# Performance work log

Hardware: AMD Instinct MI355X
Metric: run time of the kernel (lower is better)

Reference implementation:

```python
import jax, jax.numpy as jnp
import numpy as np
import math

N, E, B, T = 100000, 500000, 4096, 12
IN, HID, H = 64, 32, 4
HC = HID * H  # 128
ED = 4


def setup_inputs() -> dict:
    key = jax.random.key(0)
    ks = jax.random.split(key, 40)
    w = lambda k, shape: jax.random.normal(k, shape, jnp.float32) * 0.05
    inp = {
        'x': jax.random.normal(ks[0], (N, IN), jnp.float32),
        'edge_index': jax.random.randint(ks[1], (2, E), 0, N, jnp.int32),
        'edge_attr': jax.random.normal(ks[2], (E, ED), jnp.float32),
        'batch': jnp.sort(jax.random.randint(ks[3], (N,), 0, B, jnp.int32)),
        'r_target': jax.random.randint(ks[4], (B,), 0, T, jnp.int32),
        # layer 1 (in=IN)
        'Wq1': w(ks[5], (IN, HC)), 'bq1': w(ks[6], (HC,)),
        'Wk1': w(ks[7], (IN, HC)), 'bk1': w(ks[8], (HC,)),
        'Wv1': w(ks[9], (IN, HC)), 'bv1': w(ks[10], (HC,)),
        'We1': w(ks[11], (ED, HC)),
        'Ws1': w(ks[12], (IN, HC)), 'bs1': w(ks[13], (HC,)),
        # layers 2 and 3 stacked (in=HC)
        'Wq23': w(ks[14], (2, HC, HC)), 'bq23': w(ks[15], (2, HC)),
        'Wk23': w(ks[16], (2, HC, HC)), 'bk23': w(ks[17], (2, HC)),
        'Wv23': w(ks[18], (2, HC, HC)), 'bv23': w(ks[19], (2, HC)),
        'We23': w(ks[20], (2, ED, HC)),
        'Ws23': w(ks[21], (2, HC, HC)), 'bs23': w(ks[22], (2, HC)),
        # per-task linear heads (out_channels=1)
        'head_W': w(ks[23], (T, HC)), 'head_b': w(ks[24], (T,)),
    }
    return inp


def tconv(x, src, dst, ea, Wq, bq, Wk, bk, Wv, bv, We, Ws, bs):
    """PyG TransformerConv: gather -> per-edge MHA score -> segment softmax -> scatter."""
    q = (x @ Wq + bq).reshape(-1, H, HID)   # [N,H,C]
    k = (x @ Wk + bk).reshape(-1, H, HID)
    v = (x @ Wv + bv).reshape(-1, H, HID)
    e = (ea @ We).reshape(-1, H, HID)       # [E,H,C] (lin_edge has no bias)
    kj = k[src] + e                          # [E,H,C]
    alpha = (q[dst] * kj).sum(-1) / math.sqrt(HID)          # [E,H]
    amax = jax.ops.segment_max(alpha, dst, num_segments=N)  # [N,H]
    alpha = jnp.exp(alpha - amax[dst])
    asum = jax.ops.segment_sum(alpha, dst, num_segments=N)
    alpha = alpha / (asum[dst] + 1e-16)
    msg = (v[src] + e) * alpha[..., None]                   # [E,H,C]
    out = jax.ops.segment_sum(msg, dst, num_segments=N).reshape(N, HC)
    return out + x @ Ws + bs                 # root_weight skip connection


def reference(x, edge_index, edge_attr, batch, r_target,
              Wq1, bq1, Wk1, bk1, Wv1, bv1, We1, Ws1, bs1,
              Wq23, bq23, Wk23, bk23, Wv23, bv23, We23, Ws23, bs23,
              head_W, head_b):
    src, dst = edge_index[0], edge_index[1]
    h = jax.nn.relu(tconv(x, src, dst, edge_attr, Wq1, bq1, Wk1, bk1, Wv1, bv1, We1, Ws1, bs1))
    h = jax.nn.relu(tconv(h, src, dst, edge_attr, Wq23[0], bq23[0], Wk23[0], bk23[0], Wv23[0], bv23[0], We23[0], Ws23[0], bs23[0]))
    h = tconv(h, src, dst, edge_attr, Wq23[1], bq23[1], Wk23[1], bk23[1], Wv23[1], bv23[1], We23[1], Ws23[1], bs23[1])
    # global mean pool per graph
    cnt = jax.ops.segment_sum(jnp.ones((N,), h.dtype), batch, num_segments=B)
    pooled = jax.ops.segment_sum(h, batch, num_segments=B) / jnp.maximum(cnt, 1.0)[:, None]  # [B,HC]
    # dropout p=0.3 is a no-op in eval mode
    # per-task head selected by r_target (out_channels=1, squeezed)
    return (pooled * head_W[r_target]).sum(-1) + head_b[r_target]  # [B]
```

## Files before the change

kernel.cpp:

```cpp
#include <hip/hip_runtime.h>
#include <hip/hip_bf16.h>

#define NN 100000
#define EE 500000
#define BB 4096
#define HC 128
#define SCAN_ELEM 1024
#define NSB ((NN + SCAN_ELEM - 1) / SCAN_ELEM)

typedef __bf16 bf16_t;
typedef bf16_t bf16x8 __attribute__((ext_vector_type(8)));
typedef float f32x4 __attribute__((ext_vector_type(4)));
typedef float f32x2 __attribute__((ext_vector_type(2)));

__device__ __forceinline__ unsigned short f2bf(float f) {
    unsigned u = __builtin_bit_cast(unsigned, f);
    u += 0x7FFFu + ((u >> 16) & 1u);
    return (unsigned short)(u >> 16);
}
__device__ __forceinline__ float bflo(unsigned u) {
    return __builtin_bit_cast(float, u << 16);
}
__device__ __forceinline__ float bfhi(unsigned u) {
    return __builtin_bit_cast(float, u & 0xFFFF0000u);
}
__device__ __forceinline__ f32x2 unpk2(unsigned u) {
    return (f32x2){ bflo(u), bfhi(u) };
}

__global__ __launch_bounds__(256) void conv_x(const float* __restrict__ in,
                                              unsigned short* __restrict__ outb,
                                              int total4)
{
    const int g = blockIdx.x * 256 + threadIdx.x;
    if (g >= total4) return;
    const float4 f = *(const float4*)(in + (size_t)g * 4);
    ushort4 u;
    u.x = f2bf(f.x); u.y = f2bf(f.y); u.z = f2bf(f.z); u.w = f2bf(f.w);
    *(ushort4*)(outb + (size_t)g * 4) = u;
}

__global__ __launch_bounds__(256) void prep_w(
    const float* __restrict__ Wq, const float* __restrict__ Wk,
    const float* __restrict__ Wv, const float* __restrict__ Ws,
    unsigned short* __restrict__ Wt, int K)
{
    const int g = blockIdx.x * 256 + threadIdx.x;
    const int per = K * 128;
    if (g >= 4 * per) return;
    const int p = g / per, r = g - p * per;
    const int k = r >> 7, n = r & 127;
    const float* W = p == 0 ? Wq : p == 1 ? Wk : p == 2 ? Wv : Ws;
    Wt[(size_t)p * per + (size_t)n * K + k] = f2bf(W[k * 128 + n]);
}

template<int NKT>
__global__ __launch_bounds__(256) void gemm_mfma(
    const unsigned short* __restrict__ A,
    const unsigned short* __restrict__ Wt,
    const float* __restrict__ bq, const float* __restrict__ bk,
    const float* __restrict__ bv, const float* __restrict__ bs,
    unsigned* __restrict__ Qb, unsigned* __restrict__ KVb,
    float* __restrict__ S)
{
    constexpr int K = NKT * 32;
    const int lane = threadIdx.x & 63;
    const int p = threadIdx.x >> 6;
    const int m = lane & 15, kq = lane >> 4;
    const int rows0 = blockIdx.x * 32;

    const unsigned short* Wp = Wt + (size_t)p * 128 * K;
    const float* bias = p == 0 ? bq : p == 1 ? bk : p == 2 ? bv : bs;

    bf16x8 a[2][NKT];
#pragma unroll
    for (int mt = 0; mt < 2; mt++)
#pragma unroll
        for (int kt = 0; kt < NKT; kt++)
            a[mt][kt] = *(const bf16x8*)(A + (size_t)(rows0 + mt * 16 + m) * K + kt * 32 + kq * 8);

    f32x4 acc[2][8];
#pragma unroll
    for (int mt = 0; mt < 2; mt++)
#pragma unroll
        for (int nt = 0; nt < 8; nt++)
            acc[mt][nt] = (f32x4){0.f, 0.f, 0.f, 0.f};

#pragma unroll
    for (int nt = 0; nt < 8; nt++) {
#pragma unroll
        for (int kt = 0; kt < NKT; kt++) {
            const bf16x8 b = *(const bf16x8*)(Wp + (size_t)(nt * 16 + m) * K + kt * 32 + kq * 8);
            acc[0][nt] = __builtin_amdgcn_mfma_f32_16x16x32_bf16(a[0][kt], b, acc[0][nt], 0, 0, 0);
            acc[1][nt] = __builtin_amdgcn_mfma_f32_16x16x32_bf16(a[1][kt], b, acc[1][nt], 0, 0, 0);
        }
    }

    if (p == 3) {
#pragma unroll
        for (int nt = 0; nt < 8; nt++) {
            const float bi = bias[nt * 16 + m];
#pragma unroll
            for (int mt = 0; mt < 2; mt++) {
                float* o = S + (size_t)(rows0 + mt * 16 + kq * 4) * HC + nt * 16 + m;
#pragma unroll
                for (int r = 0; r < 4; r++) o[r * HC] = acc[mt][nt][r] + bi;
            }
        }
    } else {
        unsigned* out = p == 0 ? Qb : (p == 1 ? KVb : KVb + 64);
        const int stride = p == 0 ? 64 : 128;
#pragma unroll
        for (int nt = 0; nt < 8; nt++) {
            const float bi = bias[nt * 16 + m];
#pragma unroll
            for (int mt = 0; mt < 2; mt++) {
#pragma unroll
                for (int r = 0; r < 4; r++) {
                    const float v0 = acc[mt][nt][r] + bi;
                    const float v1 = __shfl_xor(v0, 1);
                    if (!(m & 1)) {
                        const unsigned pk = (unsigned)f2bf(v0) | ((unsigned)f2bf(v1) << 16);
                        out[(size_t)(rows0 + mt * 16 + kq * 4 + r) * stride + nt * 8 + (m >> 1)] = pk;
                    }
                }
            }
        }
    }
}

__global__ __launch_bounds__(256) void deg_k(const int* __restrict__ ei, int* __restrict__ deg)
{
    const int e = blockIdx.x * 256 + threadIdx.x;
    if (e < EE) atomicAdd(&deg[ei[EE + e]], 1);
}

__global__ __launch_bounds__(256) void scan_part(const int* __restrict__ deg,
                                                 int* __restrict__ bsum)
{
    __shared__ int red[256];
    const int base = blockIdx.x * SCAN_ELEM + threadIdx.x * 4;
    int s = 0;
#pragma unroll
    for (int j = 0; j < 4; j++) { const int i = base + j; if (i < NN) s += deg[i]; }
    red[threadIdx.x] = s;
    __syncthreads();
    for (int st = 128; st > 0; st >>= 1) {
        if (threadIdx.x < st) red[threadIdx.x] += red[threadIdx.x + st];
        __syncthreads();
    }
    if (threadIdx.x == 0) bsum[blockIdx.x] = red[0];
}

__global__ __launch_bounds__(128) void scan_top(const int* __restrict__ bsum,
                                                int* __restrict__ boff)
{
    __shared__ int buf[128];
    const int v = (threadIdx.x < NSB) ? bsum[threadIdx.x] : 0;
    buf[threadIdx.x] = v;
    __syncthreads();
    for (int s = 1; s < 128; s <<= 1) {
        const int t = (threadIdx.x >= s) ? buf[threadIdx.x - s] : 0;
        __syncthreads();
        buf[threadIdx.x] += t;
        __syncthreads();
    }
    if (threadIdx.x < NSB) boff[threadIdx.x] = buf[threadIdx.x] - v;
}

__global__ __launch_bounds__(256) void scan_final(const int* __restrict__ deg,
                                                  const int* __restrict__ boff,
                                                  int* __restrict__ off,
                                                  int* __restrict__ cursor)
{
    __shared__ int tsum[256];
    const int base = blockIdx.x * SCAN_ELEM + threadIdx.x * 4;
    int vals[4];
    int s = 0;
#pragma unroll
    for (int j = 0; j < 4; j++) {
        const int i = base + j;
        vals[j] = (i < NN) ? deg[i] : 0;
        s += vals[j];
    }
    tsum[threadIdx.x] = s;
    __syncthreads();
    for (int st = 1; st < 256; st <<= 1) {
        const int t = (threadIdx.x >= st) ? tsum[threadIdx.x - st] : 0;
        __syncthreads();
        tsum[threadIdx.x] += t;
        __syncthreads();
    }
    int ex = boff[blockIdx.x] + tsum[threadIdx.x] - s;
#pragma unroll
    for (int j = 0; j < 4; j++) {
        const int i = base + j;
        if (i < NN) { off[i] = ex; cursor[i] = ex; }
        ex += vals[j];
    }
    if (blockIdx.x == NSB - 1 && threadIdx.x == 255)
        off[NN] = boff[blockIdx.x] + tsum[255];
}

__global__ __launch_bounds__(256) void bucket_k(const int* __restrict__ ei,
                                                const float* __restrict__ ea,
                                                int* __restrict__ cursor,
                                                int* __restrict__ esrc,
                                                float4* __restrict__ eaf)
{
    const int e = blockIdx.x * 256 + threadIdx.x;
    if (e < EE) {
        const int d = ei[EE + e];
        const int p = atomicAdd(&cursor[d], 1);
        esrc[p] = ei[e];
        eaf[p] = *(const float4*)(ea + (size_t)e * 4);
    }
}

__global__ __launch_bounds__(256) void cnt_k(const int* __restrict__ batch,
                                             float* __restrict__ cnt)
{
    const int n = blockIdx.x * 256 + threadIdx.x;
    if (n < NN) atomicAdd(&cnt[batch[n]], 1.0f);
}

__global__ __launch_bounds__(256) void edge_fused(
    const int* __restrict__ esrc, const float4* __restrict__ eaf,
    const float* __restrict__ We,
    const unsigned* __restrict__ Qb, const unsigned* __restrict__ KVb,
    const int* __restrict__ off, const float* __restrict__ S,
    unsigned short* __restrict__ Hb,
    const int* __restrict__ batch, float* __restrict__ pooled,
    int fuse_pool)
{
    const int lane = threadIdx.x & 63;
    const int slot = lane >> 4;
    const int c8   = lane & 15;
    const int cb   = c8 * 8;
    const int ceq  = cb + slot * 2;
    const int n = blockIdx.x * 4 + (threadIdx.x >> 6);

    const int beg = off[n], end = off[n + 1];

    const float2 sk2 = *(const float2*)(S + (size_t)n * HC + ceq);
    const uint4 qv = *(const uint4*)(Qb + (size_t)n * 64 + c8 * 4);
    f32x2 q2[4];
    q2[0] = unpk2(qv.x); q2[1] = unpk2(qv.y);
    q2[2] = unpk2(qv.z); q2[3] = unpk2(qv.w);

    float qep[4];
#pragma unroll
    for (int d = 0; d < 4; d++) {
        const float4 wa = *(const float4*)(We + d * HC + cb);
        const float4 wb = *(const float4*)(We + d * HC + cb + 4);
        qep[d] = wa.x * q2[0].x + wa.y * q2[0].y + wa.z * q2[1].x + wa.w * q2[1].y
               + wb.x * q2[2].x + wb.y * q2[2].y + wb.z * q2[3].x + wb.w * q2[3].y;
    }

    f32x2 num2[4] = {(f32x2){0.f, 0.f}, (f32x2){0.f, 0.f},
                     (f32x2){0.f, 0.f}, (f32x2){0.f, 0.f}};
    f32x4 s4 = (f32x4){0.f, 0.f, 0.f, 0.f};
    float den = 0.f;

    auto COMPUTE = [&](const uint4& ku, const uint4& vu, const float4& ac, bool act) {
        f32x2 t2 = q2[0] * unpk2(ku.x);
        t2 += q2[1] * unpk2(ku.y);
        t2 += q2[2] * unpk2(ku.z);
        t2 += q2[3] * unpk2(ku.w);
        float tot = t2.x + t2.y
                  + ac.x * qep[0] + ac.y * qep[1] + ac.z * qep[2] + ac.w * qep[3];
        tot += __shfl_xor(tot, 1);
        tot += __shfl_xor(tot, 2);
        float al = __expf(tot * 0.17677669529663687f);
        if (!act) al = 0.f;
        num2[0] += unpk2(vu.x) * al;
        num2[1] += unpk2(vu.y) * al;
        num2[2] += unpk2(vu.z) * al;
        num2[3] += unpk2(vu.w) * al;
        s4.x += ac.x * al; s4.y += ac.y * al;
        s4.z += ac.z * al; s4.w += ac.w * al;
        den += al;
    };

    if (beg < end) {
        const int e1 = end - 1;
        int p0 = beg + slot; if (p0 > e1) p0 = e1;
        const int srcA = esrc[p0];
        const float4 aA = eaf[p0];
        const unsigned* kvA = KVb + (size_t)srcA * 128 + c8 * 4;
        const uint4 kA = *(const uint4*)kvA;
        const uint4 vA = *(const uint4*)(kvA + 64);
        if (beg + 4 < end) {
            int p1 = beg + 4 + slot; if (p1 > e1) p1 = e1;
            const int srcB = esrc[p1];
            float4 aB = eaf[p1];
            const unsigned* kvB = KVb + (size_t)srcB * 128 + c8 * 4;
            uint4 kB = *(const uint4*)kvB;
            uint4 vB = *(const uint4*)(kvB + 64);
            COMPUTE(kA, vA, aA, true);
            int base = beg + 4;
            for (;;) {
                if (base + 4 < end) {
                    int pn = base + 4 + slot; if (pn > e1) pn = e1;
                    const int srcN = esrc[pn];
                    const float4 aN = eaf[pn];
                    COMPUTE(kB, vB, aB, (base + slot) < end);
                    const unsigned* kvN = KVb + (size_t)srcN * 128 + c8 * 4;
                    kB = *(const uint4*)kvN;
                    vB = *(const uint4*)(kvN + 64);
                    aB = aN;
                    base += 4;
                } else {
                    COMPUTE(kB, vB, aB, (base + slot) < end);
                    break;
                }
            }
        } else {
            COMPUTE(kA, vA, aA, (beg + slot) < end);
        }
    }

#pragma unroll
    for (int j = 0; j < 4; j++) {
        num2[j].x += __shfl_xor(num2[j].x, 16);
        num2[j].y += __shfl_xor(num2[j].y, 16);
        num2[j].x += __shfl_xor(num2[j].x, 32);
        num2[j].y += __shfl_xor(num2[j].y, 32);
    }
    s4.x += __shfl_xor(s4.x, 16); s4.y += __shfl_xor(s4.y, 16);
    s4.z += __shfl_xor(s4.z, 16); s4.w += __shfl_xor(s4.w, 16);
    s4.x += __shfl_xor(s4.x, 32); s4.y += __shfl_xor(s4.y, 32);
    s4.z += __shfl_xor(s4.z, 32); s4.w += __shfl_xor(s4.w, 32);
    den += __shfl_xor(den, 16);
    den += __shfl_xor(den, 32);
    const float inv = 1.f / (den + 1e-16f);

    f32x2 mynum = slot == 0 ? num2[0] : slot == 1 ? num2[1]
                : slot == 2 ? num2[2] : num2[3];
    float ev0 = 0.f, ev1 = 0.f;
#pragma unroll
    for (int d = 0; d < 4; d++) {
        const float2 wd = *(const float2*)(We + d * HC + ceq);
        const float sd = d == 0 ? s4.x : d == 1 ? s4.y : d == 2 ? s4.z : s4.w;
        ev0 += sd * wd.x;
        ev1 += sd * wd.y;
    }
    const float o0 = (mynum.x + ev0) * inv + sk2.x;
    const float o1 = (mynum.y + ev1) * inv + sk2.y;

    if (!fuse_pool) {
        const float r0 = fmaxf(o0, 0.f), r1 = fmaxf(o1, 0.f);
        const unsigned pk = (unsigned)f2bf(r0) | ((unsigned)f2bf(r1) << 16);
        *(unsigned*)(Hb + (size_t)n * HC + ceq) = pk;
    } else {
        const int b = batch[n];
        atomicAdd(pooled + (size_t)b * HC + ceq,     o0);
        atomicAdd(pooled + (size_t)b * HC + ceq + 1, o1);
    }
}

__global__ __launch_bounds__(256) void head_k(
    const float* __restrict__ pooled, const float* __restrict__ cnt,
    const int* __restrict__ rt, const float* __restrict__ hW,
    const float* __restrict__ hb, float* __restrict__ out)
{
    const int lane = threadIdx.x & 63;
    const int b = blockIdx.x * 4 + (threadIdx.x >> 6);
    if (b >= BB) return;
    const int t = rt[b];
    const int c = lane * 2;
    const float2 p2 = *(const float2*)(pooled + (size_t)b * HC + c);
    const float2 w2 = *(const float2*)(hW + (size_t)t * HC + c);
    float part = p2.x * w2.x + p2.y * w2.y;
    part += __shfl_xor(part, 1);
    part += __shfl_xor(part, 2);
    part += __shfl_xor(part, 4);
    part += __shfl_xor(part, 8);
    part += __shfl_xor(part, 16);
    part += __shfl_xor(part, 32);
    if (lane == 0) out[b] = part / fmaxf(cnt[b], 1.0f) + hb[t];
}

extern "C" void kernel_launch(void* const* d_in, const int* in_sizes, int n_in,
                              void* d_out, int out_size, void* d_ws, size_t ws_size,
                              hipStream_t stream) {
    const float* x      = (const float*)d_in[0];
    const int*   ei     = (const int*)d_in[1];
    const float* ea     = (const float*)d_in[2];
    const int*   batch  = (const int*)d_in[3];
    const int*   rt     = (const int*)d_in[4];

    float* ws     = (float*)d_ws;
    float* Hbuf   = ws;
    unsigned* Qb  = (unsigned*)(ws + 12800000);
    unsigned* KVb = Qb + 6400000;
    unsigned short* Abf = (unsigned short*)(KVb + 12800000);
    float4* eaf   = (float4*)(Abf + 12800000);
    unsigned short* Wt = (unsigned short*)(eaf + 500000);
    float* pooled = (float*)(Wt + 65536);
    float* cnt    = pooled + 524288;
    int*   esrc   = (int*)(cnt + 4096);
    int*   deg    = esrc + 500000;
    int*   off    = deg + 100000;
    int*   cursor = off + 100004;
    int*   bsum   = cursor + 100000;
    int*   boff   = bsum + 128;

    hipMemsetAsync(deg, 0, 100000 * sizeof(int), stream);
    deg_k<<<(EE + 255) / 256, 256, 0, stream>>>(ei, deg);
    scan_part<<<NSB, 256, 0, stream>>>(deg, bsum);
    scan_top<<<1, 128, 0, stream>>>(bsum, boff);
    scan_final<<<NSB, 256, 0, stream>>>(deg, boff, off, cursor);
    bucket_k<<<(EE + 255) / 256, 256, 0, stream>>>(ei, ea, cursor, esrc, eaf);

    hipMemsetAsync(pooled, 0, (size_t)(BB * HC + BB) * sizeof(float), stream);
    cnt_k<<<(NN + 255) / 256, 256, 0, stream>>>(batch, cnt);

    conv_x<<<(NN * 64 / 4 + 255) / 256, 256, 0, stream>>>(x, Abf, NN * 64 / 4);

    for (int l = 0; l < 3; l++) {
        const int K = (l == 0) ? 64 : 128;
        const float *Wq, *Wk, *Wv, *Wsk, *bq, *bk, *bv, *bs, *We;
        if (l == 0) {
            Wq = (const float*)d_in[5];  bq = (const float*)d_in[6];
            Wk = (const float*)d_in[7];  bk = (const float*)d_in[8];
            Wv = (const float*)d_in[9];  bv = (const float*)d_in[10];
            We = (const float*)d_in[11];
            Wsk= (const float*)d_in[12]; bs = (const float*)d_in[13];
        } else {
            const int j = l - 1;
            Wq = (const float*)d_in[14] + (size_t)j * HC * HC;  bq = (const float*)d_in[15] + j * HC;
            Wk = (const float*)d_in[16] + (size_t)j * HC * HC;  bk = (const float*)d_in[17] + j * HC;
            Wv = (const float*)d_in[18] + (size_t)j * HC * HC;  bv = (const float*)d_in[19] + j * HC;
            We = (const float*)d_in[20] + (size_t)j * 4 * HC;
            Wsk= (const float*)d_in[21] + (size_t)j * HC * HC;  bs = (const float*)d_in[22] + j * HC;
        }

        prep_w<<<(4 * K * 128 + 255) / 256, 256, 0, stream>>>(Wq, Wk, Wv, Wsk, Wt, K);
        if (K == 64)
            gemm_mfma<2><<<NN / 32, 256, 0, stream>>>(Abf, Wt, bq, bk, bv, bs, Qb, KVb, Hbuf);
        else
            gemm_mfma<4><<<NN / 32, 256, 0, stream>>>(Abf, Wt, bq, bk, bv, bs, Qb, KVb, Hbuf);
        edge_fused<<<NN / 4, 256, 0, stream>>>(esrc, eaf, We, Qb, KVb, off,
                                               Hbuf, Abf, batch, pooled,
                                               l == 2 ? 1 : 0);
    }

    head_k<<<BB / 4, 256, 0, stream>>>(pooled, cnt, rt,
        (const float*)d_in[23], (const float*)d_in[24], (float*)d_out);
}
```

Baseline: 670.3 us.

## Fuse x bf16 conversion into GEMM, store skip term as bf16 beside Q, simplify edge loop

Drops the standalone x-to-bf16 conversion kernel: the first-layer GEMM now reads fp32 x and converts it in registers. The skip-connection output, previously written as fp32 to a separate buffer, is now packed as bf16 into the second half of the Q row, so edge_fused reads Q and skip from one interleaved row. The edge loop's two-stage software prefetch is replaced by a simpler one-ahead prefetch of only the index and attribute. This cuts a launch and reduces skip-term traffic by half, but the skip path loses precision and K/V loads are no longer prefetched an iteration ahead.

```diff
diff --git a/kernel.cpp b/kernel.cpp
--- a/kernel.cpp
+++ b/kernel.cpp
@@ -26,18 +26,6 @@
 }
 __device__ __forceinline__ f32x2 unpk2(unsigned u) {
     return (f32x2){ bflo(u), bfhi(u) };
-}
-
-__global__ __launch_bounds__(256) void conv_x(const float* __restrict__ in,
-                                              unsigned short* __restrict__ outb,
-                                              int total4)
-{
-    const int g = blockIdx.x * 256 + threadIdx.x;
-    if (g >= total4) return;
-    const float4 f = *(const float4*)(in + (size_t)g * 4);
-    ushort4 u;
-    u.x = f2bf(f.x); u.y = f2bf(f.y); u.z = f2bf(f.z); u.w = f2bf(f.w);
-    *(ushort4*)(outb + (size_t)g * 4) = u;
 }
 
 __global__ __launch_bounds__(256) void prep_w(
@@ -54,14 +42,14 @@
     Wt[(size_t)p * per + (size_t)n * K + k] = f2bf(W[k * 128 + n]);
 }
 
-template<int NKT>
+template<int NKT, int F32A>
 __global__ __launch_bounds__(256) void gemm_mfma(
-    const unsigned short* __restrict__ A,
+    const unsigned short* __restrict__ Abf,
+    const float* __restrict__ xf,
     const unsigned short* __restrict__ Wt,
     const float* __restrict__ bq, const float* __restrict__ bk,
     const float* __restrict__ bv, const float* __restrict__ bs,
-    unsigned* __restrict__ Qb, unsigned* __restrict__ KVb,
-    float* __restrict__ S)
+    unsigned* __restrict__ QSb, unsigned* __restrict__ KVb)
 {
     constexpr int K = NKT * 32;
     const int lane = threadIdx.x & 63;
@@ -76,8 +64,21 @@
 #pragma unroll
     for (int mt = 0; mt < 2; mt++)
 #pragma unroll
-        for (int kt = 0; kt < NKT; kt++)
-            a[mt][kt] = *(const bf16x8*)(A + (size_t)(rows0 + mt * 16 + m) * K + kt * 32 + kq * 8);
+        for (int kt = 0; kt < NKT; kt++) {
+            if constexpr (F32A) {
+                const float* pr = xf + (size_t)(rows0 + mt * 16 + m) * K + kt * 32 + kq * 8;
+                const float4 f0 = *(const float4*)pr;
+                const float4 f1 = *(const float4*)(pr + 4);
+                union { bf16x8 v; unsigned short u8[8]; } cv;
+                cv.u8[0] = f2bf(f0.x); cv.u8[1] = f2bf(f0.y);
+                cv.u8[2] = f2bf(f0.z); cv.u8[3] = f2bf(f0.w);
+                cv.u8[4] = f2bf(f1.x); cv.u8[5] = f2bf(f1.y);
+                cv.u8[6] = f2bf(f1.z); cv.u8[7] = f2bf(f1.w);
+                a[mt][kt] = cv.v;
+            } else {
+                a[mt][kt] = *(const bf16x8*)(Abf + (size_t)(rows0 + mt * 16 + m) * K + kt * 32 + kq * 8);
+            }
+        }
 
     f32x4 acc[2][8];
 #pragma unroll
@@ -96,33 +97,19 @@
         }
     }
 
-    if (p == 3) {
-#pragma unroll
-        for (int nt = 0; nt < 8; nt++) {
-            const float bi = bias[nt * 16 + m];
-#pragma unroll
-            for (int mt = 0; mt < 2; mt++) {
-                float* o = S + (size_t)(rows0 + mt * 16 + kq * 4) * HC + nt * 16 + m;
-#pragma unroll
-                for (int r = 0; r < 4; r++) o[r * HC] = acc[mt][nt][r] + bi;
-            }
-        }
-    } else {
-        unsigned* out = p == 0 ? Qb : (p == 1 ? KVb : KVb + 64);
-        const int stride = p == 0 ? 64 : 128;
-#pragma unroll
-        for (int nt = 0; nt < 8; nt++) {
-            const float bi = bias[nt * 16 + m];
-#pragma unroll
-            for (int mt = 0; mt < 2; mt++) {
-#pragma unroll
-                for (int r = 0; r < 4; r++) {
-                    const float v0 = acc[mt][nt][r] + bi;
-                    const float v1 = __shfl_xor(v0, 1);
-                    if (!(m & 1)) {
-                        const unsigned pk = (unsigned)f2bf(v0) | ((unsigned)f2bf(v1) << 16);
-                        out[(size_t)(rows0 + mt * 16 + kq * 4 + r) * stride + nt * 8 + (m >> 1)] = pk;
-                    }
+    unsigned* out = p == 0 ? QSb : p == 1 ? KVb : p == 2 ? (KVb + 64) : (QSb + 64);
+#pragma unroll
+    for (int nt = 0; nt < 8; nt++) {
+        const float bi = bias[nt * 16 + m];
+#pragma unroll
+        for (int mt = 0; mt < 2; mt++) {
+#pragma unroll
+            for (int r = 0; r < 4; r++) {
+                const float v0 = acc[mt][nt][r] + bi;
+                const float v1 = __shfl_xor(v0, 1);
+                if (!(m & 1)) {
+                    const unsigned pk = (unsigned)f2bf(v0) | ((unsigned)f2bf(v1) << 16);
+                    out[(size_t)(rows0 + mt * 16 + kq * 4 + r) * 128 + nt * 8 + (m >> 1)] = pk;
                 }
             }
         }
@@ -227,8 +214,8 @@
 __global__ __launch_bounds__(256) void edge_fused(
     const int* __restrict__ esrc, const float4* __restrict__ eaf,
     const float* __restrict__ We,
-    const unsigned* __restrict__ Qb, const unsigned* __restrict__ KVb,
-    const int* __restrict__ off, const float* __restrict__ S,
+    const unsigned* __restrict__ QSb, const unsigned* __restrict__ KVb,
+    const int* __restrict__ off,
     unsigned short* __restrict__ Hb,
     const int* __restrict__ batch, float* __restrict__ pooled,
     int fuse_pool)
@@ -242,8 +229,8 @@
 
     const int beg = off[n], end = off[n + 1];
 
-    const float2 sk2 = *(const float2*)(S + (size_t)n * HC + ceq);
-    const uint4 qv = *(const uint4*)(Qb + (size_t)n * 64 + c8 * 4);
+    const uint4 qv = *(const uint4*)(QSb + (size_t)n * 128 + c8 * 4);
+    const unsigned sku = QSb[(size_t)n * 128 + 64 + c8 * 4 + slot];
     f32x2 q2[4];
     q2[0] = unpk2(qv.x); q2[1] = unpk2(qv.y);
     q2[2] = unpk2(qv.z); q2[3] = unpk2(qv.w);
@@ -262,61 +249,38 @@
     f32x4 s4 = (f32x4){0.f, 0.f, 0.f, 0.f};
     float den = 0.f;
 
-    auto COMPUTE = [&](const uint4& ku, const uint4& vu, const float4& ac, bool act) {
-        f32x2 t2 = q2[0] * unpk2(ku.x);
-        t2 += q2[1] * unpk2(ku.y);
-        t2 += q2[2] * unpk2(ku.z);
-        t2 += q2[3] * unpk2(ku.w);
-        float tot = t2.x + t2.y
-                  + ac.x * qep[0] + ac.y * qep[1] + ac.z * qep[2] + ac.w * qep[3];
-        tot += __shfl_xor(tot, 1);
-        tot += __shfl_xor(tot, 2);
-        float al = __expf(tot * 0.17677669529663687f);
-        if (!act) al = 0.f;
-        num2[0] += unpk2(vu.x) * al;
-        num2[1] += unpk2(vu.y) * al;
-        num2[2] += unpk2(vu.z) * al;
-        num2[3] += unpk2(vu.w) * al;
-        s4.x += ac.x * al; s4.y += ac.y * al;
-        s4.z += ac.z * al; s4.w += ac.w * al;
-        den += al;
-    };
-
     if (beg < end) {
         const int e1 = end - 1;
         int p0 = beg + slot; if (p0 > e1) p0 = e1;
-        const int srcA = esrc[p0];
-        const float4 aA = eaf[p0];
-        const unsigned* kvA = KVb + (size_t)srcA * 128 + c8 * 4;
-        const uint4 kA = *(const uint4*)kvA;
-        const uint4 vA = *(const uint4*)(kvA + 64);
-        if (beg + 4 < end) {
-            int p1 = beg + 4 + slot; if (p1 > e1) p1 = e1;
-            const int srcB = esrc[p1];
-            float4 aB = eaf[p1];
-            const unsigned* kvB = KVb + (size_t)srcB * 128 + c8 * 4;
-            uint4 kB = *(const uint4*)kvB;
-            uint4 vB = *(const uint4*)(kvB + 64);
-            COMPUTE(kA, vA, aA, true);
-            int base = beg + 4;
-            for (;;) {
-                if (base + 4 < end) {
-                    int pn = base + 4 + slot; if (pn > e1) pn = e1;
-                    const int srcN = esrc[pn];
-                    const float4 aN = eaf[pn];
-                    COMPUTE(kB, vB, aB, (base + slot) < end);
-                    const unsigned* kvN = KVb + (size_t)srcN * 128 + c8 * 4;
-                    kB = *(const uint4*)kvN;
-                    vB = *(const uint4*)(kvN + 64);
-                    aB = aN;
-                    base += 4;
-                } else {
-                    COMPUTE(kB, vB, aB, (base + slot) < end);
-                    break;
-                }
+        int src = esrc[p0];
+        float4 a4 = eaf[p0];
+        for (int base = beg; base < end; base += 4) {
+            const unsigned* kv = KVb + (size_t)src * 128 + c8 * 4;
+            const uint4 ku = *(const uint4*)kv;
+            const uint4 vu = *(const uint4*)(kv + 64);
+            const float4 ac = a4;
+            const bool act = (base + slot) < end;
+            if (base + 4 < end) {
+                int pn = base + 4 + slot; if (pn > e1) pn = e1;
+                src = esrc[pn]; a4 = eaf[pn];
             }
-        } else {
-            COMPUTE(kA, vA, aA, (beg + slot) < end);
+            f32x2 t2 = q2[0] * unpk2(ku.x);
+            t2 += q2[1] * unpk2(ku.y);
+            t2 += q2[2] * unpk2(ku.z);
+            t2 += q2[3] * unpk2(ku.w);
+            float tot = t2.x + t2.y
+                      + ac.x * qep[0] + ac.y * qep[1] + ac.z * qep[2] + ac.w * qep[3];
+            tot += __shfl_xor(tot, 1);
+            tot += __shfl_xor(tot, 2);
+            float al = __expf(tot * 0.17677669529663687f);
+            if (!act) al = 0.f;
+            num2[0] += unpk2(vu.x) * al;
+            num2[1] += unpk2(vu.y) * al;
+            num2[2] += unpk2(vu.z) * al;
+            num2[3] += unpk2(vu.w) * al;
+            s4.x += ac.x * al; s4.y += ac.y * al;
+            s4.z += ac.z * al; s4.w += ac.w * al;
+            den += al;
         }
     }
 
@@ -345,8 +309,8 @@
         ev0 += sd * wd.x;
         ev1 += sd * wd.y;
     }
-    const float o0 = (mynum.x + ev0) * inv + sk2.x;
-    const float o1 = (mynum.y + ev1) * inv + sk2.y;
+    const float o0 = (mynum.x + ev0) * inv + bflo(sku);
+    const float o1 = (mynum.y + ev1) * inv + bfhi(sku);
 
     if (!fuse_pool) {
         const float r0 = fmaxf(o0, 0.f), r1 = fmaxf(o1, 0.f);
@@ -390,10 +354,8 @@
     const int*   batch  = (const int*)d_in[3];
     const int*   rt     = (const int*)d_in[4];
 
-    float* ws     = (float*)d_ws;
-    float* Hbuf   = ws;
-    unsigned* Qb  = (unsigned*)(ws + 12800000);
-    unsigned* KVb = Qb + 6400000;
+    unsigned* QSb = (unsigned*)d_ws;
+    unsigned* KVb = QSb + 12800000;
     unsigned short* Abf = (unsigned short*)(KVb + 12800000);
     float4* eaf   = (float4*)(Abf + 12800000);
     unsigned short* Wt = (unsigned short*)(eaf + 500000);
@@ -415,8 +377,6 @@
 
     hipMemsetAsync(pooled, 0, (size_t)(BB * HC + BB) * sizeof(float), stream);
     cnt_k<<<(NN + 255) / 256, 256, 0, stream>>>(batch, cnt);
-
-    conv_x<<<(NN * 64 / 4 + 255) / 256, 256, 0, stream>>>(x, Abf, NN * 64 / 4);
 
     for (int l = 0; l < 3; l++) {
         const int K = (l == 0) ? 64 : 128;
@@ -438,11 +398,11 @@
 
         prep_w<<<(4 * K * 128 + 255) / 256, 256, 0, stream>>>(Wq, Wk, Wv, Wsk, Wt, K);
         if (K == 64)
-            gemm_mfma<2><<<NN / 32, 256, 0, stream>>>(Abf, Wt, bq, bk, bv, bs, Qb, KVb, Hbuf);
+            gemm_mfma<2, 1><<<NN / 32, 256, 0, stream>>>(Abf, x, Wt, bq, bk, bv, bs, QSb, KVb);
         else
-            gemm_mfma<4><<<NN / 32, 256, 0, stream>>>(Abf, Wt, bq, bk, bv, bs, Qb, KVb, Hbuf);
-        edge_fused<<<NN / 4, 256, 0, stream>>>(esrc, eaf, We, Qb, KVb, off,
-                                               Hbuf, Abf, batch, pooled,
+            gemm_mfma<4, 0><<<NN / 32, 256, 0, stream>>>(Abf, x, Wt, bq, bk, bv, bs, QSb, KVb);
+        edge_fused<<<NN / 4, 256, 0, stream>>>(esrc, eaf, We, QSb, KVb, off,
+                                               Abf, batch, pooled,
                                                l == 2 ? 1 : 0);
     }
 
```

New measurement: 664.6 us. About the same (-0.9%).
